# Optimization experiments

Hardware: AMD Instinct MI355X
Metric: run time of the kernel (lower is better)

The kernel has to match this reference:

```python
import jax, jax.numpy as jnp
import numpy as np

B, S, D_IN, H, D_OUT = 128, 2048, 256, 256, 256
FORECAST = 1

def setup_inputs() -> dict:
    key = jax.random.key(0)
    ks = jax.random.split(key, 20)
    def lin(k, o, i):
        bound = 1.0 / np.sqrt(i)
        return jax.random.uniform(k, (o, i), jnp.float32, -bound, bound)
    def bias(k, o, i):
        bound = 1.0 / np.sqrt(i)
        return jax.random.uniform(k, (o,), jnp.float32, -bound, bound)
    inp = {
        "x": jax.random.normal(ks[0], (B, S, D_IN), jnp.float32),
        # layer 0 (input_size -> hidden)
        "Wf0": lin(ks[1], H, D_IN), "bf0": bias(ks[2], H, D_IN), "Uf0": lin(ks[3], H, H),
        "Wi0": lin(ks[4], H, D_IN), "bi0": bias(ks[5], H, D_IN), "Ui0": lin(ks[6], H, H),
        "Wx0": lin(ks[7], H, D_IN), "bx0": bias(ks[8], H, D_IN),
        # layer 1 (hidden -> hidden)
        "Wf1": lin(ks[9], H, H), "bf1": bias(ks[10], H, H), "Uf1": lin(ks[11], H, H),
        "Wi1": lin(ks[12], H, H), "bi1": bias(ks[13], H, H), "Ui1": lin(ks[14], H, H),
        "Wx1": lin(ks[15], H, H), "bx1": bias(ks[16], H, H),
        # output head
        "fcW": lin(ks[17], D_OUT, H), "fcb": bias(ks[18], D_OUT, H),
    }
    return inp

def _ran_layer(xseq, Wf, bf, Uf, Wi, bi, Ui, Wx, bx):
    # xseq: [B, S, D]. Precompute all input projections in three batched GEMMs,
    # then scan only the recurrent part (h @ U.T + gates + elementwise update).
    xf = jnp.einsum('bsd,hd->bsh', xseq, Wf) + bf  # [B,S,H]
    xi = jnp.einsum('bsd,hd->bsh', xseq, Wi) + bi
    xp = jnp.einsum('bsd,hd->bsh', xseq, Wx) + bx
    def step(h, inp):
        xf_t, xi_t, xp_t = inp                      # each [B,H]
        f = jax.nn.sigmoid(xf_t + h @ Uf.T)
        i = jax.nn.sigmoid(xi_t + h @ Ui.T)
        h = f * h + i * xp_t
        return h, h
    h0 = jnp.zeros((xseq.shape[0], Uf.shape[0]), xseq.dtype)
    seq = (jnp.swapaxes(xf, 0, 1), jnp.swapaxes(xi, 0, 1), jnp.swapaxes(xp, 0, 1))
    _, hs = jax.lax.scan(step, h0, seq)             # hs: [S,B,H]
    return jnp.swapaxes(hs, 0, 1)                   # [B,S,H]

def reference(x, Wf0, bf0, Uf0, Wi0, bi0, Ui0, Wx0, bx0,
              Wf1, bf1, Uf1, Wi1, bi1, Ui1, Wx1, bx1, fcW, fcb):
    h1 = _ran_layer(x,  Wf0, bf0, Uf0, Wi0, bi0, Ui0, Wx0, bx0)
    h2 = _ran_layer(h1, Wf1, bf1, Uf1, Wi1, bi1, Ui1, Wx1, bx1)
    # dropout in eval mode == identity; take last FORECAST steps then fc
    out = h2[:, -FORECAST:, :]                      # [B,FORECAST,H]
    return jnp.einsum('bth,oh->bto', out, fcW) + fcb
```

## Files before the change

### kernel.cpp

```cpp
#include <hip/hip_runtime.h>
#include <hip/hip_bf16.h>
#include <cstdint>
#include <cstddef>


typedef __bf16 bf16;
typedef __bf16 bf16x8 __attribute__((ext_vector_type(8)));
typedef __bf16 bf16x4 __attribute__((ext_vector_type(4)));
typedef __bf16 bf16x2 __attribute__((ext_vector_type(2)));
typedef float  floatx4 __attribute__((ext_vector_type(4)));

#define B_   128
#define S_   2048
#define H_   256
#define NEG_LOG2E -1.442695040888963f
#define NGB  160
#define SMEM_BYTES (84 * 1024)

__global__ void prep_weights(
    const float* __restrict__ Wf0, const float* __restrict__ Wi0, const float* __restrict__ Wx0,
    const float* __restrict__ Wf1, const float* __restrict__ Wi1, const float* __restrict__ Wx1,
    const float* __restrict__ Uf0, const float* __restrict__ Ui0,
    const float* __restrict__ Uf1, const float* __restrict__ Ui1,
    const float* __restrict__ bf0, const float* __restrict__ bi0, const float* __restrict__ bx0,
    const float* __restrict__ bf1, const float* __restrict__ bi1, const float* __restrict__ bx1,
    const float* __restrict__ fcW,
    bf16* __restrict__ W0cat, bf16* __restrict__ W1cat,
    bf16* __restrict__ U0cat, bf16* __restrict__ U1cat,
    float* __restrict__ b0cat, float* __restrict__ b1cat, float* __restrict__ fcWT)
{
    int tid = blockIdx.x * blockDim.x + threadIdx.x;
    int nth = gridDim.x * blockDim.x;
    for (int idx = tid; idx < 768 * 256; idx += nth) {
        int r = idx >> 8, k = idx & 255, rr = r & 255;
        const float* s0 = (r < 256) ? Wf0 : ((r < 512) ? Wi0 : Wx0);
        const float* s1 = (r < 256) ? Wf1 : ((r < 512) ? Wi1 : Wx1);
        W0cat[idx] = (bf16)s0[rr * 256 + k];
        W1cat[idx] = (bf16)s1[rr * 256 + k];
    }
    for (int idx = tid; idx < 512 * 256; idx += nth) {
        int r = idx >> 8, k = idx & 255, rr = r & 255;
        U0cat[idx] = (bf16)((r < 256 ? Uf0 : Ui0)[rr * 256 + k]);
        U1cat[idx] = (bf16)((r < 256 ? Uf1 : Ui1)[rr * 256 + k]);
    }
    for (int idx = tid; idx < 768; idx += nth) {
        const float* s0 = (idx < 256) ? bf0 : ((idx < 512) ? bi0 : bx0);
        const float* s1 = (idx < 256) ? bf1 : ((idx < 512) ? bi1 : bx1);
        b0cat[idx] = s0[idx & 255];
        b1cat[idx] = s1[idx & 255];
    }
    for (int idx = tid; idx < 256 * 256; idx += nth) {
        int h = idx >> 8, o = idx & 255;
        fcWT[idx] = fcW[o * 256 + h];
    }
}

__global__ void convert_x(const float* __restrict__ x, bf16* __restrict__ xa, int t0, int T)
{
    int tid = blockIdx.x * blockDim.x + threadIdx.x;
    int d4 = tid & 63;
    int b  = (tid >> 6) & 127;
    int t  = tid >> 13;
    if (t >= T) return;
    const float4* src = (const float4*)(x + ((size_t)b * S_ + t0 + t) * H_) + d4;
    float4 v = *src;
    bf16x4 o = { (bf16)v.x, (bf16)v.y, (bf16)v.z, (bf16)v.w };
    *((bf16x4*)(xa + ((size_t)t * B_ + b) * H_) + d4) = o;
}

__device__ __forceinline__ void gemm_tile(
    char* smem,
    const bf16* __restrict__ Abase,
    const bf16* __restrict__ W, const float* __restrict__ bias,
    float* __restrict__ preP, int t, int nb)
{
    bf16* At = (bf16*)smem;
    bf16* Bt = (bf16*)smem + 128 * 32;
    int n0 = nb * 128;
    int tid = threadIdx.x;
    int lane = tid & 63, wave = tid >> 6;
    int wm = (wave >> 2) * 64, wn = (wave & 3) * 32;
    int qm = lane & 15, qk = lane >> 4;
    floatx4 acc[4][2] = {};

    for (int k0 = 0; k0 < 256; k0 += 32) {
        {
            int c = tid, row = c >> 2, kc = c & 3;
            *(bf16x8*)(At + c * 8) = *(const bf16x8*)(Abase + (size_t)row * 256 + k0 + kc * 8);
            *(bf16x8*)(Bt + c * 8) = *(const bf16x8*)(W + (size_t)(n0 + row) * 256 + k0 + kc * 8);
        }
        __syncthreads();
        bf16x8 af[4], bfr[2];
#pragma unroll
        for (int i = 0; i < 4; ++i)
            af[i] = *(const bf16x8*)(At + (wm + i * 16 + qm) * 32 + qk * 8);
#pragma unroll
        for (int n = 0; n < 2; ++n)
            bfr[n] = *(const bf16x8*)(Bt + (wn + n * 16 + qm) * 32 + qk * 8);
#pragma unroll
        for (int mi = 0; mi < 4; ++mi)
#pragma unroll
            for (int ni = 0; ni < 2; ++ni)
                acc[mi][ni] = __builtin_amdgcn_mfma_f32_16x16x32_bf16(af[mi], bfr[ni], acc[mi][ni], 0, 0, 0);
        __syncthreads();
    }
#pragma unroll
    for (int mi = 0; mi < 4; ++mi) {
        int b = wm + mi * 16 + qk * 4;
        int wgi = b >> 2;
#pragma unroll
        for (int ni = 0; ni < 2; ++ni) {
            int c = n0 + wn + ni * 16 + qm;
            int g = c >> 8;
            float bb = bias[c];
            float4 v;
            float* vp = (float*)&v;
#pragma unroll
            for (int r = 0; r < 4; ++r) {
                float val = acc[mi][ni][r] + bb;
                vp[r] = (g < 2) ? NEG_LOG2E * val : val;
            }
            *(float4*)(preP + ((size_t)t * 32 + wgi) * 3072 + (size_t)c * 4) = v;
        }
    }
}

__device__ __forceinline__ void rec_wg(
    char* smem, int wg,
    const float* __restrict__ preP,
    bf16* __restrict__ hout,
    const bf16* __restrict__ Ucat,
    float* __restrict__ hstate,
    int T)
{
    bf16* hbb = (bf16*)smem;
    const int tid = threadIdx.x, lane = tid & 63, wave = tid >> 6;
    const int qm = lane & 15, qk = lane >> 4;
    const int row = qk;
    const int colq = qm;
    const int bbase = wg * 4, cb = wave * 32;
    const bool selhi16 = (lane & 16) != 0;
    const bool selhi32 = (lane & 32) != 0;

    bf16x8 Ufr[2][8], Uir[2][8];
#pragma unroll
    for (int nt = 0; nt < 2; ++nt)
#pragma unroll
        for (int kt = 0; kt < 8; ++kt) {
            Ufr[nt][kt] = *(const bf16x8*)(Ucat + (size_t)(cb + nt * 16 + qm) * 256 + kt * 32 + qk * 8);
            Uir[nt][kt] = *(const bf16x8*)(Ucat + (size_t)(256 + cb + nt * 16 + qm) * 256 + kt * 32 + qk * 8);
        }
    {
        int r2 = tid >> 7, c2 = (tid & 127) * 2;
        const float* hs = hstate + (size_t)(bbase + r2) * 256 + c2;
        bf16x2 v = { (bf16)hs[0], (bf16)hs[1] };
        *(bf16x2*)(hbb + r2 * 272 + c2) = v;
    }
    float hm0 = hstate[(size_t)(bbase + row) * 256 + cb + colq];
    float hm1 = hstate[(size_t)(bbase + row) * 256 + cb + 16 + colq];
    __syncthreads();

    const float* pw = preP + (size_t)wg * 3072 + (size_t)((cb + colq) * 4 + row);
#define PLD(dst, tt) { size_t o_ = (size_t)(tt) * 98304;                          \
        dst[0] = pw[o_];        dst[1] = pw[o_ + 64];   dst[2] = pw[o_ + 1024];   \
        dst[3] = pw[o_ + 1088]; dst[4] = pw[o_ + 2048]; dst[5] = pw[o_ + 2112]; }

    int cur = 0;

    auto spread = [&](floatx4 v) -> float {
        float s01 = selhi16 ? v[1] : v[0];
        float s23 = selhi16 ? v[3] : v[2];
        return selhi32 ? s23 : s01;
    };

    auto step = [&](int t, const float* p) {
        floatx4 f0{}, f1{}, i0{}, i1{};
        const bf16* hc = hbb + cur * (4 * 272);
#pragma unroll
        for (int kt = 0; kt < 8; ++kt) {
            bf16x8 a = *(const bf16x8*)(hc + (qm & 3) * 272 + kt * 32 + qk * 8);
            f0 = __builtin_amdgcn_mfma_f32_16x16x32_bf16(a, Ufr[0][kt], f0, 0, 0, 0);
            f1 = __builtin_amdgcn_mfma_f32_16x16x32_bf16(a, Ufr[1][kt], f1, 0, 0, 0);
            i0 = __builtin_amdgcn_mfma_f32_16x16x32_bf16(a, Uir[0][kt], i0, 0, 0, 0);
            i1 = __builtin_amdgcn_mfma_f32_16x16x32_bf16(a, Uir[1][kt], i1, 0, 0, 0);
        }
        float zf0 = spread(f0), zf1 = spread(f1);
        float zi0 = spread(i0), zi1 = spread(i1);
        bf16* hn = hbb + (cur ^ 1) * (4 * 272);
        {
            float ef = fminf(fmaf(zf0, NEG_LOG2E, p[0]), 80.0f);
            float ei = fminf(fmaf(zi0, NEG_LOG2E, p[2]), 80.0f);
            float A1 = 1.0f + __builtin_amdgcn_exp2f(ef);
            float B1 = 1.0f + __builtin_amdgcn_exp2f(ei);
            float N  = fmaf(hm0, B1, p[4] * A1);
            hm0 = N * __builtin_amdgcn_rcpf(A1 * B1);
            hn[row * 272 + cb + colq] = (bf16)hm0;
        }
        {
            float ef = fminf(fmaf(zf1, NEG_LOG2E, p[1]), 80.0f);
            float ei = fminf(fmaf(zi1, NEG_LOG2E, p[3]), 80.0f);
            float A1 = 1.0f + __builtin_amdgcn_exp2f(ef);
            float B1 = 1.0f + __builtin_amdgcn_exp2f(ei);
            float N  = fmaf(hm1, B1, p[5] * A1);
            hm1 = N * __builtin_amdgcn_rcpf(A1 * B1);
            hn[row * 272 + cb + 16 + colq] = (bf16)hm1;
        }
        asm volatile("s_waitcnt lgkmcnt(0)\n\ts_barrier" ::: "memory");
        if (hout) {
            int r2 = tid >> 7, c2 = (tid & 127) * 2;
            bf16x2 v = *(const bf16x2*)(hn + r2 * 272 + c2);
            *(bf16x2*)(hout + ((size_t)t * 128 + bbase + r2) * 256 + c2) = v;
        }
        cur ^= 1;
    };

    float bA[6], bB[6], bC[6], bD[6];
    PLD(bA, 0);
    PLD(bB, 1);
    for (int t = 0; t < T; t += 4) {
        PLD(bC, (t + 2 < T) ? t + 2 : T - 1);
        step(t, bA);
        PLD(bD, (t + 3 < T) ? t + 3 : T - 1);
        step(t + 1, bB);
        PLD(bA, (t + 4 < T) ? t + 4 : T - 1);
        step(t + 2, bC);
        PLD(bB, (t + 5 < T) ? t + 5 : T - 1);
        step(t + 3, bD);
    }
#undef PLD
    hstate[(size_t)(bbase + row) * 256 + cb + colq]      = hm0;
    hstate[(size_t)(bbase + row) * 256 + cb + 16 + colq] = hm1;
}

__global__ __launch_bounds__(512) void mega(
    const bf16* __restrict__ xa, int t0n,
    const bf16* __restrict__ W0, const float* __restrict__ b0,
    const bf16* __restrict__ W1, const float* __restrict__ b1,
    const bf16* __restrict__ U0, const bf16* __restrict__ U1,
    float* __restrict__ h0s, float* __restrict__ h1s,
    float* __restrict__ pre0n,
    const float* __restrict__ pre0c,
    bf16*  __restrict__ h1bc,
    const bf16* __restrict__ h1bp,
    float* __restrict__ pre1p,
    const float* __restrict__ pre1pp,
    int flags, int T)
{
    __shared__ __align__(16) char smem[SMEM_BYTES];
    int bx = blockIdx.x;
    if (bx < 32) {
        if (flags & 1) rec_wg(smem, bx, pre0c, h1bc, U0, h0s, T);
        return;
    }
    if (bx < 64) {
        if (flags & 4) rec_wg(smem, bx - 32, pre1pp, nullptr, U1, h1s, T);
        return;
    }
    int ng0 = (flags & 8) ? T * 6 : 0;
    int ng1 = (flags & 2) ? T * 6 : 0;
    for (int tile = bx - 64; tile < ng0 + ng1; tile += NGB) {
        bool is0 = tile < ng0;
        int tt = is0 ? tile : tile - ng0;
        int t = tt / 6, nb = tt - t * 6;
        const bf16* A = is0 ? (xa + (size_t)(t0n + t) * 32768)
                            : (h1bp + (size_t)t * 32768);
        gemm_tile(smem, A, is0 ? W0 : W1, is0 ? b0 : b1,
                  is0 ? pre0n : pre1p, t, nb);
    }
}

__global__ void fc_head(const float* __restrict__ h2, const float* __restrict__ fcWT,
                        const float* __restrict__ fcb, float* __restrict__ out)
{
    int b = blockIdx.x, o = threadIdx.x;
    __shared__ float hrow[256];
    hrow[o] = h2[(size_t)b * 256 + o];
    __syncthreads();
    float acc = fcb[o];
#pragma unroll 8
    for (int h = 0; h < 256; ++h)
        acc = fmaf(hrow[h], fcWT[h * 256 + o], acc);
    out[(size_t)b * 256 + o] = acc;
}

extern "C" void kernel_launch(void* const* d_in, const int* in_sizes, int n_in,
                              void* d_out, int out_size, void* d_ws, size_t ws_size,
                              hipStream_t stream)
{
    (void)in_sizes; (void)n_in; (void)out_size;
    const float* x   = (const float*)d_in[0];
    const float* Wf0 = (const float*)d_in[1];
    const float* bf0 = (const float*)d_in[2];
    const float* Uf0 = (const float*)d_in[3];
    const float* Wi0 = (const float*)d_in[4];
    const float* bi0 = (const float*)d_in[5];
    const float* Ui0 = (const float*)d_in[6];
    const float* Wx0 = (const float*)d_in[7];
    const float* bx0 = (const float*)d_in[8];
    const float* Wf1 = (const float*)d_in[9];
    const float* bf1 = (const float*)d_in[10];
    const float* Uf1 = (const float*)d_in[11];
    const float* Wi1 = (const float*)d_in[12];
    const float* bi1 = (const float*)d_in[13];
    const float* Ui1 = (const float*)d_in[14];
    const float* Wx1 = (const float*)d_in[15];
    const float* bx1 = (const float*)d_in[16];
    const float* fcW = (const float*)d_in[17];
    const float* fcb = (const float*)d_in[18];

    char* p = (char*)d_ws;
    auto alloc = [&](size_t bytes) -> char* {
        char* r = p; p += (bytes + 255) & ~(size_t)255; return r;
    };
    bf16*  W0cat = (bf16*)alloc(768 * 256 * 2);
    bf16*  W1cat = (bf16*)alloc(768 * 256 * 2);
    bf16*  U0cat = (bf16*)alloc(512 * 256 * 2);
    bf16*  U1cat = (bf16*)alloc(512 * 256 * 2);
    float* b0cat = (float*)alloc(768 * 4);
    float* b1cat = (float*)alloc(768 * 4);
    float* fcWT  = (float*)alloc(256 * 256 * 4);
    float* h0s   = (float*)alloc(128 * 256 * 4);
    float* h1s   = (float*)alloc(128 * 256 * 4);
    size_t fixed = (size_t)(p - (char*)d_ws);

    int T_c = 128;
    while (T_c > 32 &&
           fixed + 134217728ULL + (size_t)T_c * 1703936ULL + 4096 > ws_size)
        T_c >>= 1;
    bf16*  xa    = (bf16*)alloc((size_t)S_ * 128 * 256 * 2);
    float* pre0s[2], *pre1s[2];
    bf16*  h1bs[2];
    pre0s[0] = (float*)alloc((size_t)T_c * 128 * 768 * 4);
    pre0s[1] = (float*)alloc((size_t)T_c * 128 * 768 * 4);
    pre1s[0] = (float*)alloc((size_t)T_c * 128 * 768 * 4);
    pre1s[1] = (float*)alloc((size_t)T_c * 128 * 768 * 4);
    h1bs[0]  = (bf16*)alloc((size_t)T_c * 128 * 256 * 2);
    h1bs[1]  = (bf16*)alloc((size_t)T_c * 128 * 256 * 2);

    hipMemsetAsync(h0s, 0, 128 * 256 * 4, stream);
    hipMemsetAsync(h1s, 0, 128 * 256 * 4, stream);

    prep_weights<<<512, 256, 0, stream>>>(Wf0, Wi0, Wx0, Wf1, Wi1, Wx1,
                                          Uf0, Ui0, Uf1, Ui1,
                                          bf0, bi0, bx0, bf1, bi1, bx1, fcW,
                                          W0cat, W1cat, U0cat, U1cat, b0cat, b1cat, fcWT);
    convert_x<<<S_ * 32, 256, 0, stream>>>(x, xa, 0, S_);

    int NC = S_ / T_c;
    for (int k = -1; k <= NC + 1; ++k) {
        int flags = 0;
        if (k >= 0 && k < NC)     flags |= 1;
        if (k >= 1 && k <= NC)    flags |= 2;
        if (k >= 2 && k <= NC+1)  flags |= 4;
        if (k <= NC - 2)          flags |= 8;
        mega<<<64 + NGB, 512, 0, stream>>>(
            xa, (k + 1) * T_c,
            W0cat, b0cat, W1cat, b1cat, U0cat, U1cat, h0s, h1s,
            pre0s[(k + 1) & 1],
            pre0s[k & 1],
            h1bs[k & 1],
            h1bs[(k - 1) & 1],
            pre1s[(k - 1) & 1],
            pre1s[k & 1],
            flags, T_c);
    }
    fc_head<<<128, 256, 0, stream>>>(h1s, fcWT, fcb, (float*)d_out);
}
```

Measured before the change: 2.306 ms.

## Split recurrent batch across twice as many workgroups, two rows each

Each recurrence workgroup now handles 2 batch rows instead of 4, so 64 workgroups per layer run the serial scan instead of 32. The per-step elementwise work per thread halves and the preactivation buffer layout changes to a 2-row interleave to match. GEMM workers drop from 160 to 96 so the total grid stays within the device. Each recurrence step still issues the same MFMA count with half the rows wasted, and the smaller GEMM pool may lengthen the overlapped projection work.

```diff
diff --git a/kernel.cpp b/kernel.cpp
--- a/kernel.cpp
+++ b/kernel.cpp
@@ -14,7 +14,7 @@
 #define S_   2048
 #define H_   256
 #define NEG_LOG2E -1.442695040888963f
-#define NGB  160
+#define NGB  96
 #define SMEM_BYTES (84 * 1024)
 
 __global__ void prep_weights(
@@ -107,20 +107,21 @@
 #pragma unroll
     for (int mi = 0; mi < 4; ++mi) {
         int b = wm + mi * 16 + qk * 4;
-        int wgi = b >> 2;
+        int wgA = b >> 1;
 #pragma unroll
         for (int ni = 0; ni < 2; ++ni) {
             int c = n0 + wn + ni * 16 + qm;
             int g = c >> 8;
             float bb = bias[c];
-            float4 v;
-            float* vp = (float*)&v;
-#pragma unroll
-            for (int r = 0; r < 4; ++r) {
-                float val = acc[mi][ni][r] + bb;
-                vp[r] = (g < 2) ? NEG_LOG2E * val : val;
+            float v0 = acc[mi][ni][0] + bb, v1 = acc[mi][ni][1] + bb;
+            float v2 = acc[mi][ni][2] + bb, v3 = acc[mi][ni][3] + bb;
+            if (g < 2) {
+                v0 *= NEG_LOG2E; v1 *= NEG_LOG2E;
+                v2 *= NEG_LOG2E; v3 *= NEG_LOG2E;
             }
-            *(float4*)(preP + ((size_t)t * 32 + wgi) * 3072 + (size_t)c * 4) = v;
+            float2 w0 = { v0, v1 }, w1 = { v2, v3 };
+            *(float2*)(preP + ((size_t)t * 64 + wgA)     * 1536 + (size_t)c * 2) = w0;
+            *(float2*)(preP + ((size_t)t * 64 + wgA + 1) * 1536 + (size_t)c * 2) = w1;
         }
     }
 }
@@ -136,11 +137,13 @@
     bf16* hbb = (bf16*)smem;
     const int tid = threadIdx.x, lane = tid & 63, wave = tid >> 6;
     const int qm = lane & 15, qk = lane >> 4;
-    const int row = qk;
-    const int colq = qm;
-    const int bbase = wg * 4, cb = wave * 32;
-    const bool selhi16 = (lane & 16) != 0;
-    const bool selhi32 = (lane & 32) != 0;
+    const int row = qk & 1;
+    const int ch  = qk >> 1;
+    const int cb  = wave * 32;
+    const int col = cb + ch * 16 + qm;
+    const int bbase = wg * 2;
+    const bool selrow = (lane & 16) != 0;
+    const bool selch  = (lane & 32) != 0;
 
     bf16x8 Ufr[2][8], Uir[2][8];
 #pragma unroll
@@ -151,70 +154,53 @@
             Uir[nt][kt] = *(const bf16x8*)(Ucat + (size_t)(256 + cb + nt * 16 + qm) * 256 + kt * 32 + qk * 8);
         }
     {
-        int r2 = tid >> 7, c2 = (tid & 127) * 2;
-        const float* hs = hstate + (size_t)(bbase + r2) * 256 + c2;
-        bf16x2 v = { (bf16)hs[0], (bf16)hs[1] };
-        *(bf16x2*)(hbb + r2 * 272 + c2) = v;
-    }
-    float hm0 = hstate[(size_t)(bbase + row) * 256 + cb + colq];
-    float hm1 = hstate[(size_t)(bbase + row) * 256 + cb + 16 + colq];
+        int r2 = tid >> 8, c2 = tid & 255;
+        hbb[r2 * 272 + c2] = (bf16)hstate[(size_t)(bbase + r2) * 256 + c2];
+    }
+    float hm = hstate[(size_t)(bbase + row) * 256 + col];
     __syncthreads();
 
-    const float* pw = preP + (size_t)wg * 3072 + (size_t)((cb + colq) * 4 + row);
-#define PLD(dst, tt) { size_t o_ = (size_t)(tt) * 98304;                          \
-        dst[0] = pw[o_];        dst[1] = pw[o_ + 64];   dst[2] = pw[o_ + 1024];   \
-        dst[3] = pw[o_ + 1088]; dst[4] = pw[o_ + 2048]; dst[5] = pw[o_ + 2112]; }
+    const float* pw = preP + (size_t)wg * 1536 + (size_t)(col * 2 + row);
+#define PLD(dst, tt) { size_t o_ = (size_t)(tt) * 98304;                   \
+        dst[0] = pw[o_]; dst[1] = pw[o_ + 512]; dst[2] = pw[o_ + 1024]; }
 
     int cur = 0;
 
-    auto spread = [&](floatx4 v) -> float {
-        float s01 = selhi16 ? v[1] : v[0];
-        float s23 = selhi16 ? v[3] : v[2];
-        return selhi32 ? s23 : s01;
+    auto pick = [&](floatx4 v0, floatx4 v1) -> float {
+        float a0 = selrow ? v0[1] : v0[0];
+        float a1 = selrow ? v1[1] : v1[0];
+        return selch ? a1 : a0;
     };
 
     auto step = [&](int t, const float* p) {
         floatx4 f0{}, f1{}, i0{}, i1{};
-        const bf16* hc = hbb + cur * (4 * 272);
+        const bf16* hc = hbb + cur * (2 * 272);
 #pragma unroll
         for (int kt = 0; kt < 8; ++kt) {
-            bf16x8 a = *(const bf16x8*)(hc + (qm & 3) * 272 + kt * 32 + qk * 8);
+            bf16x8 a = *(const bf16x8*)(hc + (qm & 1) * 272 + kt * 32 + qk * 8);
             f0 = __builtin_amdgcn_mfma_f32_16x16x32_bf16(a, Ufr[0][kt], f0, 0, 0, 0);
             f1 = __builtin_amdgcn_mfma_f32_16x16x32_bf16(a, Ufr[1][kt], f1, 0, 0, 0);
             i0 = __builtin_amdgcn_mfma_f32_16x16x32_bf16(a, Uir[0][kt], i0, 0, 0, 0);
             i1 = __builtin_amdgcn_mfma_f32_16x16x32_bf16(a, Uir[1][kt], i1, 0, 0, 0);
         }
-        float zf0 = spread(f0), zf1 = spread(f1);
-        float zi0 = spread(i0), zi1 = spread(i1);
-        bf16* hn = hbb + (cur ^ 1) * (4 * 272);
-        {
-            float ef = fminf(fmaf(zf0, NEG_LOG2E, p[0]), 80.0f);
-            float ei = fminf(fmaf(zi0, NEG_LOG2E, p[2]), 80.0f);
-            float A1 = 1.0f + __builtin_amdgcn_exp2f(ef);
-            float B1 = 1.0f + __builtin_amdgcn_exp2f(ei);
-            float N  = fmaf(hm0, B1, p[4] * A1);
-            hm0 = N * __builtin_amdgcn_rcpf(A1 * B1);
-            hn[row * 272 + cb + colq] = (bf16)hm0;
-        }
-        {
-            float ef = fminf(fmaf(zf1, NEG_LOG2E, p[1]), 80.0f);
-            float ei = fminf(fmaf(zi1, NEG_LOG2E, p[3]), 80.0f);
-            float A1 = 1.0f + __builtin_amdgcn_exp2f(ef);
-            float B1 = 1.0f + __builtin_amdgcn_exp2f(ei);
-            float N  = fmaf(hm1, B1, p[5] * A1);
-            hm1 = N * __builtin_amdgcn_rcpf(A1 * B1);
-            hn[row * 272 + cb + 16 + colq] = (bf16)hm1;
-        }
+        float zf = pick(f0, f1), zi = pick(i0, i1);
+        bf16* hn = hbb + (cur ^ 1) * (2 * 272);
+        float ef = fminf(fmaf(zf, NEG_LOG2E, p[0]), 80.0f);
+        float ei = fminf(fmaf(zi, NEG_LOG2E, p[1]), 80.0f);
+        float A1 = 1.0f + __builtin_amdgcn_exp2f(ef);
+        float B1 = 1.0f + __builtin_amdgcn_exp2f(ei);
+        float N  = fmaf(hm, B1, p[2] * A1);
+        hm = N * __builtin_amdgcn_rcpf(A1 * B1);
+        hn[row * 272 + col] = (bf16)hm;
         asm volatile("s_waitcnt lgkmcnt(0)\n\ts_barrier" ::: "memory");
         if (hout) {
-            int r2 = tid >> 7, c2 = (tid & 127) * 2;
-            bf16x2 v = *(const bf16x2*)(hn + r2 * 272 + c2);
-            *(bf16x2*)(hout + ((size_t)t * 128 + bbase + r2) * 256 + c2) = v;
+            int r2 = tid >> 8, c2 = tid & 255;
+            hout[((size_t)t * 128 + bbase + r2) * 256 + c2] = hn[r2 * 272 + c2];
         }
         cur ^= 1;
     };
 
-    float bA[6], bB[6], bC[6], bD[6];
+    float bA[3], bB[3], bC[3], bD[3];
     PLD(bA, 0);
     PLD(bB, 1);
     for (int t = 0; t < T; t += 4) {
@@ -228,8 +214,7 @@
         step(t + 3, bD);
     }
 #undef PLD
-    hstate[(size_t)(bbase + row) * 256 + cb + colq]      = hm0;
-    hstate[(size_t)(bbase + row) * 256 + cb + 16 + colq] = hm1;
+    hstate[(size_t)(bbase + row) * 256 + col] = hm;
 }
 
 __global__ __launch_bounds__(512) void mega(
@@ -248,17 +233,17 @@
 {
     __shared__ __align__(16) char smem[SMEM_BYTES];
     int bx = blockIdx.x;
-    if (bx < 32) {
+    if (bx < 64) {
         if (flags & 1) rec_wg(smem, bx, pre0c, h1bc, U0, h0s, T);
         return;
     }
-    if (bx < 64) {
-        if (flags & 4) rec_wg(smem, bx - 32, pre1pp, nullptr, U1, h1s, T);
+    if (bx < 128) {
+        if (flags & 4) rec_wg(smem, bx - 64, pre1pp, nullptr, U1, h1s, T);
         return;
     }
     int ng0 = (flags & 8) ? T * 6 : 0;
     int ng1 = (flags & 2) ? T * 6 : 0;
-    for (int tile = bx - 64; tile < ng0 + ng1; tile += NGB) {
+    for (int tile = bx - 128; tile < ng0 + ng1; tile += NGB) {
         bool is0 = tile < ng0;
         int tt = is0 ? tile : tile - ng0;
         int t = tt / 6, nb = tt - t * 6;
@@ -353,7 +338,7 @@
         if (k >= 1 && k <= NC)    flags |= 2;
         if (k >= 2 && k <= NC+1)  flags |= 4;
         if (k <= NC - 2)          flags |= 8;
-        mega<<<64 + NGB, 512, 0, stream>>>(
+        mega<<<128 + NGB, 512, 0, stream>>>(
             xa, (k + 1) * T_c,
             W0cat, b0cat, W1cat, b1cat, U0cat, U1cat, h0s, h1s,
             pre0s[(k + 1) & 1],
```

Measured after the change: 2.329 ms. About the same (+1.0%).
